# Kernel optimization log

Measured on AMD Instinct MI355X. Metric: run time of the kernel, lower is better.

Reference implementation:

```python
import jax, jax.numpy as jnp
import numpy as np

HID = 1024; INTER = 2048; NSTATE = 16; KCONV = 4; DTRANK = 64
NHEADS = 16; NKV = 4; HDIM = 64; VHDIM = 128; EPS = 1e-6
ATTN_H = HID; K_H = NKV * HDIM; V_H = NKV * VHDIM
LATENT = INTER + ATTN_H + K_H + V_H  # 3840


def rmsnorm(x, w, eps=EPS):
    return x * jax.lax.rsqrt(jnp.mean(x * x, axis=-1, keepdims=True) + eps) * w


def setup_inputs():
    key = jax.random.key(0)
    ks = jax.random.split(key, 8)
    B, S = 2, 2048
    s = 0.02
    x = jax.random.normal(ks[0], (B, S, HID), jnp.float32)
    W_in = jax.random.normal(ks[1], (LATENT + INTER, HID), jnp.float32) * s
    conv_w = jax.random.normal(ks[2], (INTER, KCONV), jnp.float32) * 0.2
    conv_b = jnp.zeros((INTER,), jnp.float32)
    W_x = jax.random.normal(ks[3], (DTRANK + 2 * NSTATE, INTER), jnp.float32) * s
    dt_ln_w = jnp.ones((DTRANK,), jnp.float32)
    B_ln_w = jnp.ones((NSTATE,), jnp.float32)
    C_ln_w = jnp.ones((NSTATE,), jnp.float32)
    W_dt = jax.random.normal(ks[4], (INTER, DTRANK), jnp.float32) * s
    b_dt = jnp.log(jnp.expm1(jnp.full((INTER,), 0.01, jnp.float32)))
    A_log = jnp.log(jnp.broadcast_to(jnp.arange(1, NSTATE + 1, dtype=jnp.float32)[None, :], (INTER, NSTATE)))
    D_param = jnp.ones((INTER,), jnp.float32)
    ln1_w = jnp.ones((INTER,), jnp.float32)
    ln2_w = jnp.ones((INTER,), jnp.float32)
    W_out = jax.random.normal(ks[5], (HID, INTER), jnp.float32) * s
    return {"x": x, "W_in": W_in, "conv_w": conv_w, "conv_b": conv_b, "W_x": W_x,
            "dt_ln_w": dt_ln_w, "B_ln_w": B_ln_w, "C_ln_w": C_ln_w, "W_dt": W_dt,
            "b_dt": b_dt, "A_log": A_log, "D_param": D_param, "ln1_w": ln1_w,
            "ln2_w": ln2_w, "W_out": W_out}


def reference(x, W_in, conv_w, conv_b, W_x, dt_ln_w, B_ln_w, C_ln_w, W_dt, b_dt,
              A_log, D_param, ln1_w, ln2_w, W_out):
    Bsz, S, _ = x.shape
    proj = x @ W_in.T  # [B,S,LATENT+INTER]
    q = proj[..., :ATTN_H]
    k = proj[..., ATTN_H:ATTN_H + K_H]
    v = proj[..., ATTN_H + K_H:ATTN_H + K_H + V_H]
    xs = proj[..., ATTN_H + K_H + V_H:LATENT]
    gate = proj[..., LATENT:]

    # depthwise causal conv1d + silu (causal_conv1d_fn)
    xt = xs.transpose(0, 2, 1)  # [B,D,S]
    xc = jax.lax.conv_general_dilated(xt, conv_w[:, None, :], (1,), [(KCONV - 1, 0)],
                                      feature_group_count=INTER,
                                      dimension_numbers=("NCH", "OIH", "NCH"))
    xc = jax.nn.silu(xc + conv_b[None, :, None]).transpose(0, 2, 1)  # [B,S,D]

    # input-dependent dt, B, C with inner RMSNorms
    ssm_p = xc @ W_x.T  # [B,S,DTRANK+2N]
    dt = rmsnorm(ssm_p[..., :DTRANK], dt_ln_w)
    Bm = rmsnorm(ssm_p[..., DTRANK:DTRANK + NSTATE], B_ln_w)
    Cm = rmsnorm(ssm_p[..., DTRANK + NSTATE:], C_ln_w)
    delta = jax.nn.softplus(dt @ W_dt.T + b_dt)  # [B,S,D] (delta_bias + softplus)
    A = -jnp.exp(A_log)  # [D,N]

    def step(h, inp):
        d_t, b_t, c_t, x_t = inp  # [B,D],[B,N],[B,N],[B,D]
        dA = jnp.exp(d_t[:, :, None] * A)  # [B,D,N]
        h = h * dA + (d_t * x_t)[:, :, None] * b_t[:, None, :]
        y = jnp.einsum("bdn,bn->bd", h, c_t)
        return h, y

    h0 = jnp.zeros((Bsz, INTER, NSTATE), x.dtype)
    _, ys = jax.lax.scan(step, h0, (delta.transpose(1, 0, 2), Bm.transpose(1, 0, 2),
                                    Cm.transpose(1, 0, 2), xc.transpose(1, 0, 2)))
    y = ys.transpose(1, 0, 2) + xc * D_param
    y = y * jax.nn.silu(gate)  # gated scan output [B,S,INTER]

    # causal GQA attention branch (no output proj; v_head_dim = INTER/NHEADS)
    qh = q.reshape(Bsz, S, NHEADS, HDIM).transpose(0, 2, 1, 3)
    kh = jnp.repeat(k.reshape(Bsz, S, NKV, HDIM), NHEADS // NKV, axis=2).transpose(0, 2, 1, 3)
    vh = jnp.repeat(v.reshape(Bsz, S, NKV, VHDIM), NHEADS // NKV, axis=2).transpose(0, 2, 1, 3)
    scores = jnp.einsum("bhqd,bhkd->bhqk", qh, kh) * (1.0 / float(np.sqrt(HDIM)))
    mask = jnp.tril(jnp.ones((S, S), bool))
    scores = jnp.where(mask, scores, jnp.finfo(scores.dtype).min)
    attn = jnp.einsum("bhqk,bhkd->bhqd", jax.nn.softmax(scores, axis=-1), vh)
    attn = attn.transpose(0, 2, 1, 3).reshape(Bsz, S, INTER)

    out = (rmsnorm(attn, ln1_w) + rmsnorm(y, ln2_w)) * 0.5
    return out @ W_out.T
```

## Files before the change

kernel.cpp:

```cpp
#include <hip/hip_runtime.h>
#include <stdint.h>

#define HID    1024
#define INTER  2048
#define NSTATE 16
#define DTRANK 64
#define NHEADS 16
#define NKV    4
#define HDIM   64
#define VHDIM  128
#define ATTN_H 1024
#define K_H    256
#define V_H    512
#define LATENT 3840
#define NCOLS  5888
#define BATCH  2
#define SEQ    2048
#define T_TOT  4096
#define NCHUNK 64
#define CHLEN  32

typedef __bf16 bf16x8 __attribute__((ext_vector_type(8)));
typedef float  f32x4  __attribute__((ext_vector_type(4)));
typedef float  f32x4v __attribute__((ext_vector_type(4)));
typedef unsigned short u16x8 __attribute__((ext_vector_type(8)));

__device__ __forceinline__ float bf2f(unsigned short u) {
    return __uint_as_float(((unsigned int)u) << 16);
}
__device__ __forceinline__ unsigned short f2bf(float f) {
    unsigned int u = __float_as_uint(f);
    u = (u + 0x7fffu + ((u >> 16) & 1u)) >> 16;
    return (unsigned short)u;
}
__device__ __forceinline__ bf16x8 ldb8(const unsigned short* p) {
    return __builtin_bit_cast(bf16x8, *(const u16x8*)p);
}

typedef const __attribute__((address_space(1))) unsigned int* gas_ptr;
typedef __attribute__((address_space(3))) unsigned int* las_ptr;
__device__ __forceinline__ void load_lds16(const void* g, void* l) {
    __builtin_amdgcn_global_load_lds((gas_ptr)g, (las_ptr)l, 16, 0, 0);
}

__global__ void k_cvt(const float* __restrict__ src, unsigned short* __restrict__ dst, int n8) {
    int i = blockIdx.x * blockDim.x + threadIdx.x;
    if (i >= n8) return;
    f32x4v a = ((const f32x4v*)src)[2 * i];
    f32x4v b = ((const f32x4v*)src)[2 * i + 1];
    u16x8 o;
#pragma unroll
    for (int k = 0; k < 4; k++) { o[k] = f2bf(a[k]); o[k + 4] = f2bf(b[k]); }
    *(u16x8*)(dst + (size_t)i * 8) = o;
}

__global__ void k_wxpad(const float* __restrict__ W_x, unsigned short* __restrict__ Wxpad) {
    int i = blockIdx.x * blockDim.x + threadIdx.x;
    int e = i * 8;
    int row = e >> 11;
    int col = e & 2047;
    u16x8 o;
    if (row < DTRANK + 2 * NSTATE) {
#pragma unroll
        for (int k = 0; k < 8; k++) o[k] = f2bf(W_x[(size_t)row * INTER + col + k]);
    } else {
#pragma unroll
        for (int k = 0; k < 8; k++) o[k] = 0;
    }
    *(u16x8*)(Wxpad + e) = o;
}

template <int OUT_MODE>
__launch_bounds__(256)
__global__ void k_gemm(const unsigned short* __restrict__ A, const unsigned short* __restrict__ B,
                       void* __restrict__ Cout, const float* __restrict__ bias,
                       int M, int N, int K, int lda, int ldb, int ldc) {
    __shared__ __align__(16) unsigned short As[128 * 64];
    __shared__ __align__(16) unsigned short Bs[128 * 64];
    const int tid = threadIdx.x;
    const int lane = tid & 63;
    const int w = tid >> 6;
    const int wm = w >> 1, wn = w & 1;
    const int bm = blockIdx.y * 128, bn = blockIdx.x * 128;

    f32x4 acc[4][4];
#pragma unroll
    for (int i = 0; i < 4; i++)
#pragma unroll
        for (int j = 0; j < 4; j++) acc[i][j] = (f32x4){0.f, 0.f, 0.f, 0.f};

    const int nk = K >> 6;
    for (int ks = 0; ks < nk; ++ks) {
        const int k0 = ks << 6;
#pragma unroll
        for (int i = 0; i < 4; ++i) {
            int qb = (w << 6) + (i << 8);
            int q = qb + lane;
            int row = q >> 3, c = q & 7;
            int csrc = c ^ (row & 7);
            load_lds16(A + (size_t)(bm + row) * lda + k0 + csrc * 8, As + qb * 8);
            load_lds16(B + (size_t)(bn + row) * ldb + k0 + csrc * 8, Bs + qb * 8);
        }
        __syncthreads();
#pragma unroll
        for (int kk = 0; kk < 2; ++kk) {
            bf16x8 af[4], bfr[4];
#pragma unroll
            for (int mi = 0; mi < 4; mi++) {
                int row = (wm << 6) + (mi << 4) + (lane & 15);
                int c = (kk << 2) + (lane >> 4);
                af[mi] = ldb8(As + row * 64 + (c ^ (row & 7)) * 8);
            }
#pragma unroll
            for (int ni = 0; ni < 4; ni++) {
                int row = (wn << 6) + (ni << 4) + (lane & 15);
                int c = (kk << 2) + (lane >> 4);
                bfr[ni] = ldb8(Bs + row * 64 + (c ^ (row & 7)) * 8);
            }
#pragma unroll
            for (int mi = 0; mi < 4; mi++)
#pragma unroll
                for (int ni = 0; ni < 4; ni++)
                    acc[mi][ni] = __builtin_amdgcn_mfma_f32_16x16x32_bf16(af[mi], bfr[ni], acc[mi][ni], 0, 0, 0);
        }
        __syncthreads();
    }
#pragma unroll
    for (int mi = 0; mi < 4; mi++)
#pragma unroll
        for (int ni = 0; ni < 4; ni++)
#pragma unroll
            for (int r = 0; r < 4; r++) {
                int grow = bm + (wm << 6) + (mi << 4) + ((lane >> 4) << 2) + r;
                int gcol = bn + (wn << 6) + (ni << 4) + (lane & 15);
                float v = acc[mi][ni][r];
                if (OUT_MODE == 0) {
                    ((unsigned short*)Cout)[(size_t)grow * ldc + gcol] = f2bf(v);
                } else if (OUT_MODE == 1) {
                    ((float*)Cout)[(size_t)grow * ldc + gcol] = v;
                } else {
                    v += bias[gcol];
                    v = (v > 20.f) ? v : log1pf(__expf(v));
                    ((unsigned short*)Cout)[(size_t)grow * ldc + gcol] = f2bf(v);
                }
            }
}

__global__ void k_conv(const unsigned short* __restrict__ proj, const float* __restrict__ conv_w,
                       const float* __restrict__ conv_b, unsigned short* __restrict__ xc) {
    int r = blockIdx.x;
    int d8 = threadIdx.x * 8;
    int t = r & (SEQ - 1);
    float accv[8];
#pragma unroll
    for (int i = 0; i < 8; i++) accv[i] = conv_b[d8 + i];
#pragma unroll
    for (int j = 0; j < 4; j++) {
        int tp = t - 3 + j;
        if (tp < 0) continue;
        u16x8 xv = *(const u16x8*)(proj + (size_t)(r - 3 + j) * NCOLS + (LATENT - INTER) + d8);
#pragma unroll
        for (int i = 0; i < 8; i++) accv[i] += conv_w[(d8 + i) * 4 + j] * bf2f(xv[i]);
    }
    u16x8 o;
#pragma unroll
    for (int i = 0; i < 8; i++) {
        float v = accv[i];
        v = v / (1.f + __expf(-v));
        o[i] = f2bf(v);
    }
    *(u16x8*)(xc + (size_t)r * INTER + d8) = o;
}

__global__ void k_rms3(const float* __restrict__ ssmp, const float* __restrict__ dt_w,
                       const float* __restrict__ B_w, const float* __restrict__ C_w,
                       unsigned short* __restrict__ dtbf, float* __restrict__ Bm, float* __restrict__ Cm) {
    int r = blockIdx.x;
    int tid = threadIdx.x;
    int lane = tid & 63, w = tid >> 6;
    int c = tid;
    float v = (c < 96) ? ssmp[(size_t)r * 128 + c] : 0.f;
    float s = v * v;
    if (w == 0) {
#pragma unroll
        for (int d = 1; d < 64; d <<= 1) s += __shfl_xor(s, d);
        float rms = rsqrtf(s * (1.f / 64.f) + 1e-6f);
        dtbf[(size_t)r * 64 + lane] = f2bf(v * rms * dt_w[lane]);
    } else {
#pragma unroll
        for (int d = 1; d < 16; d <<= 1) s += __shfl_xor(s, d);
        float rms = rsqrtf(s * (1.f / 16.f) + 1e-6f);
        if (lane < 16) Bm[(size_t)r * 16 + lane] = v * rms * B_w[lane];
        else if (lane < 32) Cm[(size_t)r * 16 + (lane - 16)] = v * rms * C_w[lane - 16];
    }
}

template <int PASS>
__launch_bounds__(256)
__global__ void k_scan_chunk(const unsigned short* __restrict__ deltabf, const unsigned short* __restrict__ xcbf,
                             const float* __restrict__ Bm, const float* __restrict__ Cm,
                             const float* __restrict__ A_log,
                             float* __restrict__ hend, float* __restrict__ sumd,
                             const float* __restrict__ hinit, unsigned short* __restrict__ ybf) {
    __shared__ __align__(16) unsigned short dltS[CHLEN * 256];
    __shared__ __align__(16) unsigned short xvS[CHLEN * 256];
    __shared__ __align__(16) float BsT[CHLEN * 16];
    __shared__ __align__(16) float CsT[CHLEN * 16];
    const int d0 = blockIdx.x * 256;
    const int c = blockIdx.y;
    const int b = blockIdx.z;
    const int tid = threadIdx.x, lane = tid & 63, w = tid >> 6;
    const int t0 = c * CHLEN;
    const size_t rowbase = (size_t)(b * SEQ + t0);

    float An[16];
    {
        const f32x4* ap = (const f32x4*)(A_log + (size_t)(d0 + tid) * 16);
#pragma unroll
        for (int n4 = 0; n4 < 4; n4++) {
            f32x4 av = ap[n4];
#pragma unroll
            for (int j = 0; j < 4; j++) An[n4 * 4 + j] = -__expf(av[j]);
        }
    }

#pragma unroll
    for (int i = 0; i < 4; ++i) {
        int qb = (w << 6) + (i << 8);
        int q = qb + lane;
        int t = q >> 5, coff = q & 31;
        load_lds16(deltabf + (rowbase + t) * INTER + d0 + coff * 8, dltS + qb * 8);
        load_lds16(xcbf + (rowbase + t) * INTER + d0 + coff * 8, xvS + qb * 8);
    }
    if (tid < 128) {
        ((f32x4*)BsT)[tid] = ((const f32x4*)(Bm + rowbase * 16))[tid];
        if (PASS == 2) ((f32x4*)CsT)[tid] = ((const f32x4*)(Cm + rowbase * 16))[tid];
    }
    __syncthreads();

    const size_t sidx = ((size_t)(c * BATCH + b) * INTER + d0 + tid) * 16;
    float h[16];
    if (PASS == 2) {
        const f32x4* hp = (const f32x4*)(hinit + sidx);
#pragma unroll
        for (int n4 = 0; n4 < 4; n4++) {
            f32x4 hv = hp[n4];
#pragma unroll
            for (int j = 0; j < 4; j++) h[n4 * 4 + j] = hv[j];
        }
    } else {
#pragma unroll
        for (int n = 0; n < 16; n++) h[n] = 0.f;
    }
    float sd = 0.f;
    for (int t = 0; t < CHLEN; ++t) {
        float dlt = bf2f(dltS[t * 256 + tid]);
        float xv = bf2f(xvS[t * 256 + tid]);
        float dx = dlt * xv;
        if (PASS == 0) sd += dlt;
        float y = 0.f;
#pragma unroll
        for (int n4 = 0; n4 < 4; ++n4) {
            f32x4 Bt = ((f32x4*)BsT)[t * 4 + n4];
            f32x4 Ct;
            if (PASS == 2) Ct = ((f32x4*)CsT)[t * 4 + n4];
#pragma unroll
            for (int j = 0; j < 4; ++j) {
                int n = n4 * 4 + j;
                float a = __expf(dlt * An[n]);
                h[n] = h[n] * a + dx * Bt[j];
                if (PASS == 2) y += h[n] * Ct[j];
            }
        }
        if (PASS == 2) ybf[(rowbase + t) * INTER + d0 + tid] = f2bf(y);
    }
    if (PASS == 0) {
        f32x4* hp = (f32x4*)(hend + sidx);
#pragma unroll
        for (int n4 = 0; n4 < 4; n4++) {
            f32x4 hv;
#pragma unroll
            for (int j = 0; j < 4; j++) hv[j] = h[n4 * 4 + j];
            hp[n4] = hv;
        }
        sumd[(size_t)(c * BATCH + b) * INTER + d0 + tid] = sd;
    }
}

__global__ void k_scan_prop(const float* __restrict__ A_log, const float* __restrict__ hend,
                            const float* __restrict__ sumd, float* __restrict__ hinit) {
    const int tid = blockIdx.x * 256 + threadIdx.x;
    const int n = tid & 15;
    const int d = (tid >> 4) & (INTER - 1);
    const float An = -__expf(A_log[(size_t)d * 16 + n]);
    const int bd = tid >> 4;
    float h = 0.f;
#pragma unroll 1
    for (int cb = 0; cb < NCHUNK / 4; ++cb) {
        float he[4], sdv[4];
#pragma unroll
        for (int j = 0; j < 4; j++) {
            int c = cb * 4 + j;
            he[j] = hend[(size_t)c * 65536 + tid];
            sdv[j] = sumd[(size_t)c * 4096 + bd];
        }
#pragma unroll
        for (int j = 0; j < 4; j++) {
            int c = cb * 4 + j;
            hinit[(size_t)c * 65536 + tid] = h;
            h = he[j] + __expf(An * sdv[j]) * h;
        }
    }
}

__launch_bounds__(256)
__global__ void k_attn(const unsigned short* __restrict__ proj, unsigned short* __restrict__ attn) {
    __shared__ __align__(16) unsigned short Ks[64 * 72];
    __shared__ __align__(16) unsigned short Vt[128 * 72];
    __shared__ __align__(16) unsigned short Ps[4 * 16 * 72];
    const int qt = (gridDim.x - 1) - blockIdx.x;
    const int h = blockIdx.y;
    const int b = blockIdx.z;
    const int g = h >> 2;
    const int tid = threadIdx.x, lane = tid & 63, w = tid >> 6;
    const int r0 = qt * 128;
    const int qw = r0 + w * 32;

    const int krow = tid >> 3, kc = tid & 7;
    const int kp2 = (tid & 31) * 2, vb = tid >> 5;

    const unsigned short* kbase = proj + (size_t)(b * SEQ) * NCOLS + ATTN_H + g * HDIM;
    const unsigned short* vbase = proj + (size_t)(b * SEQ) * NCOLS + (ATTN_H + K_H) + g * VHDIM;

    bf16x8 qf[2][2];
#pragma unroll
    for (int f = 0; f < 2; f++) {
        int qr = qw + f * 16 + (lane & 15);
        const unsigned short* qp = proj + (size_t)(b * SEQ + qr) * NCOLS + h * HDIM + ((lane >> 4) << 3);
        qf[f][0] = ldb8(qp);
        qf[f][1] = ldb8(qp + 32);
    }
    f32x4 O[2][8];
#pragma unroll
    for (int f = 0; f < 2; f++)
#pragma unroll
        for (int vf = 0; vf < 8; vf++) O[f][vf] = (f32x4){0.f, 0.f, 0.f, 0.f};
    float l_[2][4];
#pragma unroll
    for (int f = 0; f < 2; f++)
#pragma unroll
        for (int rg = 0; rg < 4; rg++) l_[f][rg] = 0.f;

    u16x8 krA[2], vrA[2][2], krB[2], vrB[2][2];

    auto LOAD = [&](u16x8* kr, u16x8 (*vr)[2], int kv) {
        const unsigned short* kp_ = kbase + (size_t)(kv + krow) * NCOLS + kc * 8;
        kr[0] = *(const u16x8*)kp_;
        kr[1] = *(const u16x8*)(kp_ + (size_t)32 * NCOLS);
        const unsigned short* vp_ = vbase + (size_t)(kv + kp2) * NCOLS + vb * 8;
        vr[0][0] = *(const u16x8*)vp_;
        vr[0][1] = *(const u16x8*)(vp_ + NCOLS);
        vr[1][0] = *(const u16x8*)(vp_ + 64);
        vr[1][1] = *(const u16x8*)(vp_ + NCOLS + 64);
    };
    auto WRITE = [&](u16x8* kr, u16x8 (*vr)[2]) {
        *(u16x8*)&Ks[krow * 72 + kc * 8] = kr[0];
        *(u16x8*)&Ks[(krow + 32) * 72 + kc * 8] = kr[1];
#pragma unroll
        for (int hf = 0; hf < 2; hf++) {
            u16x8 va = vr[hf][0], vb2 = vr[hf][1];
#pragma unroll
            for (int i = 0; i < 8; i++) {
                unsigned int pk = (unsigned int)va[i] | ((unsigned int)vb2[i] << 16);
                *(unsigned int*)&Vt[((vb + hf * 8) * 8 + i) * 72 + kp2] = pk;
            }
        }
    };
    auto COMPUTE = [&](int kv) {
        const int pbase = w * 16 * 72;
#pragma unroll
        for (int f = 0; f < 2; f++) {
            f32x4 sv[4];
#pragma unroll
            for (int cf = 0; cf < 4; ++cf) {
                f32x4 s = (f32x4){0.f, 0.f, 0.f, 0.f};
#pragma unroll
                for (int kk = 0; kk < 2; ++kk) {
                    bf16x8 kb = ldb8(&Ks[(cf * 16 + (lane & 15)) * 72 + kk * 32 + ((lane >> 4) << 3)]);
                    s = __builtin_amdgcn_mfma_f32_16x16x32_bf16(qf[f][kk], kb, s, 0, 0, 0);
                }
                sv[cf] = s;
            }
            const int qi0 = qw + f * 16 + ((lane >> 4) << 2);
#pragma unroll
            for (int cf = 0; cf < 4; ++cf) {
                int ki = kv + cf * 16 + (lane & 15);
#pragma unroll
                for (int rg = 0; rg < 4; ++rg) {
                    float v = (ki <= qi0 + rg) ? __expf(sv[cf][rg] * 0.125f) : 0.f;
                    l_[f][rg] += v;
                    Ps[pbase + (((lane >> 4) << 2) + rg) * 72 + cf * 16 + (lane & 15)] = f2bf(v);
                }
            }
            bf16x8 pa0 = ldb8(&Ps[pbase + (lane & 15) * 72 + ((lane >> 4) << 3)]);
            bf16x8 pa1 = ldb8(&Ps[pbase + (lane & 15) * 72 + 32 + ((lane >> 4) << 3)]);
#pragma unroll
            for (int vf = 0; vf < 8; ++vf) {
                bf16x8 v0 = ldb8(&Vt[(vf * 16 + (lane & 15)) * 72 + ((lane >> 4) << 3)]);
                bf16x8 v1 = ldb8(&Vt[(vf * 16 + (lane & 15)) * 72 + 32 + ((lane >> 4) << 3)]);
                O[f][vf] = __builtin_amdgcn_mfma_f32_16x16x32_bf16(pa0, v0, O[f][vf], 0, 0, 0);
                O[f][vf] = __builtin_amdgcn_mfma_f32_16x16x32_bf16(pa1, v1, O[f][vf], 0, 0, 0);
            }
        }
    };

    const int ntiles = 2 * (qt + 1);
    LOAD(krA, vrA, 0);
    for (int jj = 0; jj < ntiles; jj += 2) {
        WRITE(krA, vrA);
        LOAD(krB, vrB, (jj + 1) * 64);
        __syncthreads();
        COMPUTE(jj * 64);
        __syncthreads();
        WRITE(krB, vrB);
        if (jj + 2 < ntiles) LOAD(krA, vrA, (jj + 2) * 64);
        __syncthreads();
        COMPUTE((jj + 1) * 64);
        __syncthreads();
    }

#pragma unroll
    for (int f = 0; f < 2; f++) {
#pragma unroll
        for (int dd = 1; dd < 16; dd <<= 1)
#pragma unroll
            for (int rg = 0; rg < 4; ++rg) l_[f][rg] += __shfl_xor(l_[f][rg], dd);
#pragma unroll
        for (int rg = 0; rg < 4; ++rg) {
            float inv = 1.f / l_[f][rg];
            int grow = b * SEQ + qw + f * 16 + ((lane >> 4) << 2) + rg;
#pragma unroll
            for (int vf = 0; vf < 8; ++vf) {
                int gcol = h * VHDIM + vf * 16 + (lane & 15);
                attn[(size_t)grow * INTER + gcol] = f2bf(O[f][vf][rg] * inv);
            }
        }
    }
}

__launch_bounds__(256)
__global__ void k_fuse(const unsigned short* __restrict__ attn, const unsigned short* __restrict__ ybf,
                       const unsigned short* __restrict__ xc, const unsigned short* __restrict__ proj,
                       const float* __restrict__ Dp, const float* __restrict__ ln1,
                       const float* __restrict__ ln2, unsigned short* __restrict__ fused) {
    __shared__ float red[8];
    int r = blockIdx.x, tid = threadIdx.x;
    int c8 = tid * 8;
    u16x8 av = *(const u16x8*)(attn + (size_t)r * INTER + c8);
    u16x8 yv8 = *(const u16x8*)(ybf + (size_t)r * INTER + c8);
    u16x8 xv8 = *(const u16x8*)(xc + (size_t)r * INTER + c8);
    u16x8 gv8 = *(const u16x8*)(proj + (size_t)r * NCOLS + LATENT + c8);
    float a_[8], y_[8];
    float ssa = 0.f, ssy = 0.f;
#pragma unroll
    for (int i = 0; i < 8; i++) {
        float a = bf2f(av[i]);
        float yv = bf2f(yv8[i]) + bf2f(xv8[i]) * Dp[c8 + i];
        float gg = bf2f(gv8[i]);
        yv *= gg / (1.f + __expf(-gg));
        a_[i] = a; y_[i] = yv;
        ssa += a * a; ssy += yv * yv;
    }
#pragma unroll
    for (int d = 1; d < 64; d <<= 1) { ssa += __shfl_xor(ssa, d); ssy += __shfl_xor(ssy, d); }
    int w = tid >> 6, lane = tid & 63;
    if (lane == 0) { red[w * 2] = ssa; red[w * 2 + 1] = ssy; }
    __syncthreads();
    ssa = red[0] + red[2] + red[4] + red[6];
    ssy = red[1] + red[3] + red[5] + red[7];
    float ra = rsqrtf(ssa * (1.f / 2048.f) + 1e-6f);
    float ry = rsqrtf(ssy * (1.f / 2048.f) + 1e-6f);
    u16x8 o;
#pragma unroll
    for (int i = 0; i < 8; i++) {
        float v = (a_[i] * ra * ln1[c8 + i] + y_[i] * ry * ln2[c8 + i]) * 0.5f;
        o[i] = f2bf(v);
    }
    *(u16x8*)(fused + (size_t)r * INTER + c8) = o;
}

extern "C" void kernel_launch(void* const* d_in, const int* in_sizes, int n_in,
                              void* d_out, int out_size, void* d_ws, size_t ws_size,
                              hipStream_t stream) {
    const float* x      = (const float*)d_in[0];
    const float* W_in   = (const float*)d_in[1];
    const float* conv_w = (const float*)d_in[2];
    const float* conv_b = (const float*)d_in[3];
    const float* W_x    = (const float*)d_in[4];
    const float* dt_w   = (const float*)d_in[5];
    const float* B_w    = (const float*)d_in[6];
    const float* C_w    = (const float*)d_in[7];
    const float* W_dt   = (const float*)d_in[8];
    const float* b_dt   = (const float*)d_in[9];
    const float* A_log  = (const float*)d_in[10];
    const float* Dp     = (const float*)d_in[11];
    const float* ln1    = (const float*)d_in[12];
    const float* ln2    = (const float*)d_in[13];
    const float* W_out  = (const float*)d_in[14];
    float* out = (float*)d_out;

    char* p = (char*)d_ws;
    auto alloc = [&](size_t bytes) -> void* {
        void* r = (void*)p;
        p += (bytes + 255) & ~(size_t)255;
        return r;
    };
    unsigned short* xbf     = (unsigned short*)alloc((size_t)T_TOT * HID * 2);
    unsigned short* Winbf   = (unsigned short*)alloc((size_t)NCOLS * HID * 2);
    unsigned short* projbf  = (unsigned short*)alloc((size_t)T_TOT * NCOLS * 2);
    unsigned short* xcbf    = (unsigned short*)alloc((size_t)T_TOT * INTER * 2);
    unsigned short* Wxpad   = (unsigned short*)alloc((size_t)128 * INTER * 2);
    float*          ssmp    = (float*)alloc((size_t)T_TOT * 128 * 4);
    unsigned short* dtbf    = (unsigned short*)alloc((size_t)T_TOT * DTRANK * 2);
    float*          Bm      = (float*)alloc((size_t)T_TOT * 16 * 4);
    float*          Cm      = (float*)alloc((size_t)T_TOT * 16 * 4);
    unsigned short* Wdtbf   = (unsigned short*)alloc((size_t)INTER * DTRANK * 2);
    unsigned short* deltabf = (unsigned short*)alloc((size_t)T_TOT * INTER * 2);
    unsigned short* ybf     = (unsigned short*)alloc((size_t)T_TOT * INTER * 2);
    unsigned short* attnbf  = (unsigned short*)alloc((size_t)T_TOT * INTER * 2);
    unsigned short* fusedbf = (unsigned short*)alloc((size_t)T_TOT * INTER * 2);
    unsigned short* Woutbf  = (unsigned short*)alloc((size_t)HID * INTER * 2);
    float*          hendws  = (float*)alloc((size_t)NCHUNK * BATCH * INTER * 16 * 4);
    float*          hinitws = (float*)alloc((size_t)NCHUNK * BATCH * INTER * 16 * 4);
    float*          sumdws  = (float*)alloc((size_t)NCHUNK * BATCH * INTER * 4);

    k_cvt<<<(T_TOT * HID / 8 + 255) / 256, 256, 0, stream>>>(x, xbf, T_TOT * HID / 8);
    k_cvt<<<(NCOLS * HID / 8 + 255) / 256, 256, 0, stream>>>(W_in, Winbf, NCOLS * HID / 8);
    k_cvt<<<(INTER * DTRANK / 8 + 255) / 256, 256, 0, stream>>>(W_dt, Wdtbf, INTER * DTRANK / 8);
    k_cvt<<<(HID * INTER / 8 + 255) / 256, 256, 0, stream>>>(W_out, Woutbf, HID * INTER / 8);
    k_wxpad<<<(128 * INTER / 8) / 256, 256, 0, stream>>>(W_x, Wxpad);

    k_gemm<0><<<dim3(NCOLS / 128, T_TOT / 128), 256, 0, stream>>>(
        xbf, Winbf, projbf, nullptr, T_TOT, NCOLS, HID, HID, HID, NCOLS);
    k_conv<<<T_TOT, 256, 0, stream>>>(projbf, conv_w, conv_b, xcbf);
    k_gemm<1><<<dim3(1, T_TOT / 128), 256, 0, stream>>>(
        xcbf, Wxpad, ssmp, nullptr, T_TOT, 128, INTER, INTER, INTER, 128);
    k_rms3<<<T_TOT, 128, 0, stream>>>(ssmp, dt_w, B_w, C_w, dtbf, Bm, Cm);
    k_gemm<2><<<dim3(INTER / 128, T_TOT / 128), 256, 0, stream>>>(
        dtbf, Wdtbf, deltabf, b_dt, T_TOT, INTER, DTRANK, DTRANK, DTRANK, INTER);
    k_scan_chunk<0><<<dim3(INTER / 256, NCHUNK, BATCH), 256, 0, stream>>>(
        deltabf, xcbf, Bm, Cm, A_log, hendws, sumdws, nullptr, nullptr);
    k_scan_prop<<<256, 256, 0, stream>>>(A_log, hendws, sumdws, hinitws);
    k_scan_chunk<2><<<dim3(INTER / 256, NCHUNK, BATCH), 256, 0, stream>>>(
        deltabf, xcbf, Bm, Cm, A_log, nullptr, nullptr, hinitws, ybf);
    k_attn<<<dim3(SEQ / 128, NHEADS, BATCH), 256, 0, stream>>>(projbf, attnbf);
    k_fuse<<<T_TOT, 256, 0, stream>>>(attnbf, ybf, xcbf, projbf, Dp, ln1, ln2, fusedbf);
    k_gemm<1><<<dim3(HID / 128, T_TOT / 128), 256, 0, stream>>>(
        fusedbf, Woutbf, out, nullptr, T_TOT, HID, INTER, INTER, INTER, HID);
}
```

Baseline: 467.2 us.

## Split-K the x_proj GEMM and pair causal attention tiles per block

The thin x_proj GEMM (N=128, K=2048), which launched only 32 blocks, now runs as an 8-way split-K. Each split writes fp32 partials that the RMS-norm kernel sums. Attention now uses 64-row query tiles, and each block handles a complementary pair (31-p and p) so causal work is balanced across blocks. LDS K, V and P tiles switch from padded strides to XOR-swizzled layouts, and the softmax uses exp2 with a prescaled constant. The costs are extra partial-sum memory traffic and a smaller per-wave query tile.

```diff
diff --git a/kernel.cpp b/kernel.cpp
--- a/kernel.cpp
+++ b/kernel.cpp
@@ -82,6 +82,7 @@
     const int w = tid >> 6;
     const int wm = w >> 1, wn = w & 1;
     const int bm = blockIdx.y * 128, bn = blockIdx.x * 128;
+    const size_t koff = (OUT_MODE == 3) ? (size_t)blockIdx.z * K : 0;
 
     f32x4 acc[4][4];
 #pragma unroll
@@ -98,8 +99,8 @@
             int q = qb + lane;
             int row = q >> 3, c = q & 7;
             int csrc = c ^ (row & 7);
-            load_lds16(A + (size_t)(bm + row) * lda + k0 + csrc * 8, As + qb * 8);
-            load_lds16(B + (size_t)(bn + row) * ldb + k0 + csrc * 8, Bs + qb * 8);
+            load_lds16(A + (size_t)(bm + row) * lda + koff + k0 + csrc * 8, As + qb * 8);
+            load_lds16(B + (size_t)(bn + row) * ldb + koff + k0 + csrc * 8, Bs + qb * 8);
         }
         __syncthreads();
 #pragma unroll
@@ -138,6 +139,8 @@
                     ((unsigned short*)Cout)[(size_t)grow * ldc + gcol] = f2bf(v);
                 } else if (OUT_MODE == 1) {
                     ((float*)Cout)[(size_t)grow * ldc + gcol] = v;
+                } else if (OUT_MODE == 3) {
+                    ((float*)Cout)[(size_t)blockIdx.z * M * ldc + (size_t)grow * ldc + gcol] = v;
                 } else {
                     v += bias[gcol];
                     v = (v > 20.f) ? v : log1pf(__expf(v));
@@ -179,7 +182,11 @@
     int tid = threadIdx.x;
     int lane = tid & 63, w = tid >> 6;
     int c = tid;
-    float v = (c < 96) ? ssmp[(size_t)r * 128 + c] : 0.f;
+    float v = 0.f;
+    if (c < 96) {
+#pragma unroll
+        for (int s = 0; s < 8; s++) v += ssmp[(size_t)s * (T_TOT * 128) + (size_t)r * 128 + c];
+    }
     float s = v * v;
     if (w == 0) {
 #pragma unroll
@@ -315,41 +322,21 @@
 
 __launch_bounds__(256)
 __global__ void k_attn(const unsigned short* __restrict__ proj, unsigned short* __restrict__ attn) {
-    __shared__ __align__(16) unsigned short Ks[64 * 72];
-    __shared__ __align__(16) unsigned short Vt[128 * 72];
-    __shared__ __align__(16) unsigned short Ps[4 * 16 * 72];
-    const int qt = (gridDim.x - 1) - blockIdx.x;
+    __shared__ __align__(16) unsigned short Ks[64 * 64];
+    __shared__ __align__(16) unsigned short Vt[128 * 64];
+    __shared__ __align__(16) unsigned short Ps[4 * 16 * 64];
+    const int pair = blockIdx.x;
     const int h = blockIdx.y;
     const int b = blockIdx.z;
     const int g = h >> 2;
     const int tid = threadIdx.x, lane = tid & 63, w = tid >> 6;
-    const int r0 = qt * 128;
-    const int qw = r0 + w * 32;
+    const int l15 = lane & 15, hi = lane >> 4;
 
     const int krow = tid >> 3, kc = tid & 7;
     const int kp2 = (tid & 31) * 2, vb = tid >> 5;
 
     const unsigned short* kbase = proj + (size_t)(b * SEQ) * NCOLS + ATTN_H + g * HDIM;
     const unsigned short* vbase = proj + (size_t)(b * SEQ) * NCOLS + (ATTN_H + K_H) + g * VHDIM;
-
-    bf16x8 qf[2][2];
-#pragma unroll
-    for (int f = 0; f < 2; f++) {
-        int qr = qw + f * 16 + (lane & 15);
-        const unsigned short* qp = proj + (size_t)(b * SEQ + qr) * NCOLS + h * HDIM + ((lane >> 4) << 3);
-        qf[f][0] = ldb8(qp);
-        qf[f][1] = ldb8(qp + 32);
-    }
-    f32x4 O[2][8];
-#pragma unroll
-    for (int f = 0; f < 2; f++)
-#pragma unroll
-        for (int vf = 0; vf < 8; vf++) O[f][vf] = (f32x4){0.f, 0.f, 0.f, 0.f};
-    float l_[2][4];
-#pragma unroll
-    for (int f = 0; f < 2; f++)
-#pragma unroll
-        for (int rg = 0; rg < 4; rg++) l_[f][rg] = 0.f;
 
     u16x8 krA[2], vrA[2][2], krB[2], vrB[2][2];
 
@@ -364,85 +351,107 @@
         vr[1][1] = *(const u16x8*)(vp_ + NCOLS + 64);
     };
     auto WRITE = [&](u16x8* kr, u16x8 (*vr)[2]) {
-        *(u16x8*)&Ks[krow * 72 + kc * 8] = kr[0];
-        *(u16x8*)&Ks[(krow + 32) * 72 + kc * 8] = kr[1];
+        int ksw = (kc ^ (krow & 7)) << 3;
+        *(u16x8*)&Ks[krow * 64 + ksw] = kr[0];
+        *(u16x8*)&Ks[(krow + 32) * 64 + ksw] = kr[1];
 #pragma unroll
         for (int hf = 0; hf < 2; hf++) {
             u16x8 va = vr[hf][0], vb2 = vr[hf][1];
 #pragma unroll
             for (int i = 0; i < 8; i++) {
                 unsigned int pk = (unsigned int)va[i] | ((unsigned int)vb2[i] << 16);
-                *(unsigned int*)&Vt[((vb + hf * 8) * 8 + i) * 72 + kp2] = pk;
+                int r = (vb + hf * 8) * 8 + i;
+                *(unsigned int*)&Vt[r * 64 + (((kp2 >> 3) ^ (r & 7)) << 3) + (kp2 & 7)] = pk;
             }
         }
     };
-    auto COMPUTE = [&](int kv) {
-        const int pbase = w * 16 * 72;
-#pragma unroll
-        for (int f = 0; f < 2; f++) {
+
+    const float SC = 0.18033688f;
+
+    for (int phase = 0; phase < 2; ++phase) {
+        const int qt = (phase == 0) ? (31 - pair) : pair;
+        const int qw = qt * 64 + w * 16;
+        const int ntiles = qt + 1;
+
+        bf16x8 qf[2];
+        {
+            int qr = qw + l15;
+            const unsigned short* qp = proj + (size_t)(b * SEQ + qr) * NCOLS + h * HDIM + hi * 8;
+            qf[0] = ldb8(qp);
+            qf[1] = ldb8(qp + 32);
+        }
+        f32x4 O[8];
+#pragma unroll
+        for (int vf = 0; vf < 8; vf++) O[vf] = (f32x4){0.f, 0.f, 0.f, 0.f};
+        float l_[4] = {0.f, 0.f, 0.f, 0.f};
+
+        auto COMPUTE = [&](int kv) {
+            const int pbase = w * 1024;
             f32x4 sv[4];
 #pragma unroll
             for (int cf = 0; cf < 4; ++cf) {
                 f32x4 s = (f32x4){0.f, 0.f, 0.f, 0.f};
+                int row = cf * 16 + l15;
 #pragma unroll
                 for (int kk = 0; kk < 2; ++kk) {
-                    bf16x8 kb = ldb8(&Ks[(cf * 16 + (lane & 15)) * 72 + kk * 32 + ((lane >> 4) << 3)]);
-                    s = __builtin_amdgcn_mfma_f32_16x16x32_bf16(qf[f][kk], kb, s, 0, 0, 0);
+                    bf16x8 kb = ldb8(&Ks[row * 64 + ((((kk << 2) + hi) ^ (row & 7)) << 3)]);
+                    s = __builtin_amdgcn_mfma_f32_16x16x32_bf16(qf[kk], kb, s, 0, 0, 0);
                 }
                 sv[cf] = s;
             }
-            const int qi0 = qw + f * 16 + ((lane >> 4) << 2);
+            const int qi0 = qw + (hi << 2);
 #pragma unroll
             for (int cf = 0; cf < 4; ++cf) {
-                int ki = kv + cf * 16 + (lane & 15);
+                int ki = kv + cf * 16 + l15;
 #pragma unroll
                 for (int rg = 0; rg < 4; ++rg) {
-                    float v = (ki <= qi0 + rg) ? __expf(sv[cf][rg] * 0.125f) : 0.f;
-                    l_[f][rg] += v;
-                    Ps[pbase + (((lane >> 4) << 2) + rg) * 72 + cf * 16 + (lane & 15)] = f2bf(v);
+                    float v = (ki <= qi0 + rg) ? exp2f(sv[cf][rg] * SC) : 0.f;
+                    l_[rg] += v;
+                    int pr = (hi << 2) + rg;
+                    int pc = cf * 16 + l15;
+                    Ps[pbase + pr * 64 + (((pc >> 3) ^ (pr & 7)) << 3) + (pc & 7)] = f2bf(v);
                 }
             }
-            bf16x8 pa0 = ldb8(&Ps[pbase + (lane & 15) * 72 + ((lane >> 4) << 3)]);
-            bf16x8 pa1 = ldb8(&Ps[pbase + (lane & 15) * 72 + 32 + ((lane >> 4) << 3)]);
+            bf16x8 pa0 = ldb8(&Ps[pbase + l15 * 64 + ((hi ^ (l15 & 7)) << 3)]);
+            bf16x8 pa1 = ldb8(&Ps[pbase + l15 * 64 + (((4 + hi) ^ (l15 & 7)) << 3)]);
 #pragma unroll
             for (int vf = 0; vf < 8; ++vf) {
-                bf16x8 v0 = ldb8(&Vt[(vf * 16 + (lane & 15)) * 72 + ((lane >> 4) << 3)]);
-                bf16x8 v1 = ldb8(&Vt[(vf * 16 + (lane & 15)) * 72 + 32 + ((lane >> 4) << 3)]);
-                O[f][vf] = __builtin_amdgcn_mfma_f32_16x16x32_bf16(pa0, v0, O[f][vf], 0, 0, 0);
-                O[f][vf] = __builtin_amdgcn_mfma_f32_16x16x32_bf16(pa1, v1, O[f][vf], 0, 0, 0);
-            }
-        }
-    };
-
-    const int ntiles = 2 * (qt + 1);
-    LOAD(krA, vrA, 0);
-    for (int jj = 0; jj < ntiles; jj += 2) {
-        WRITE(krA, vrA);
-        LOAD(krB, vrB, (jj + 1) * 64);
-        __syncthreads();
-        COMPUTE(jj * 64);
-        __syncthreads();
-        WRITE(krB, vrB);
-        if (jj + 2 < ntiles) LOAD(krA, vrA, (jj + 2) * 64);
-        __syncthreads();
-        COMPUTE((jj + 1) * 64);
-        __syncthreads();
-    }
-
-#pragma unroll
-    for (int f = 0; f < 2; f++) {
+                int vr_ = vf * 16 + l15;
+                bf16x8 v0 = ldb8(&Vt[vr_ * 64 + ((hi ^ (vr_ & 7)) << 3)]);
+                bf16x8 v1 = ldb8(&Vt[vr_ * 64 + (((4 + hi) ^ (vr_ & 7)) << 3)]);
+                O[vf] = __builtin_amdgcn_mfma_f32_16x16x32_bf16(pa0, v0, O[vf], 0, 0, 0);
+                O[vf] = __builtin_amdgcn_mfma_f32_16x16x32_bf16(pa1, v1, O[vf], 0, 0, 0);
+            }
+        };
+
+        LOAD(krA, vrA, 0);
+        bool useA = true;
+        for (int j = 0; j < ntiles; ++j) {
+            if (useA) {
+                WRITE(krA, vrA);
+                if (j + 1 < ntiles) LOAD(krB, vrB, (j + 1) * 64);
+            } else {
+                WRITE(krB, vrB);
+                if (j + 1 < ntiles) LOAD(krA, vrA, (j + 1) * 64);
+            }
+            __syncthreads();
+            COMPUTE(j * 64);
+            __syncthreads();
+            useA = !useA;
+        }
+
 #pragma unroll
         for (int dd = 1; dd < 16; dd <<= 1)
 #pragma unroll
-            for (int rg = 0; rg < 4; ++rg) l_[f][rg] += __shfl_xor(l_[f][rg], dd);
+            for (int rg = 0; rg < 4; ++rg) l_[rg] += __shfl_xor(l_[rg], dd);
 #pragma unroll
         for (int rg = 0; rg < 4; ++rg) {
-            float inv = 1.f / l_[f][rg];
-            int grow = b * SEQ + qw + f * 16 + ((lane >> 4) << 2) + rg;
+            float inv = 1.f / l_[rg];
+            int grow = b * SEQ + qw + (hi << 2) + rg;
 #pragma unroll
             for (int vf = 0; vf < 8; ++vf) {
-                int gcol = h * VHDIM + vf * 16 + (lane & 15);
-                attn[(size_t)grow * INTER + gcol] = f2bf(O[f][vf][rg] * inv);
+                int gcol = h * VHDIM + vf * 16 + l15;
+                attn[(size_t)grow * INTER + gcol] = f2bf(O[vf][rg] * inv);
             }
         }
     }
@@ -520,7 +529,7 @@
     unsigned short* projbf  = (unsigned short*)alloc((size_t)T_TOT * NCOLS * 2);
     unsigned short* xcbf    = (unsigned short*)alloc((size_t)T_TOT * INTER * 2);
     unsigned short* Wxpad   = (unsigned short*)alloc((size_t)128 * INTER * 2);
-    float*          ssmp    = (float*)alloc((size_t)T_TOT * 128 * 4);
+    float*          ssmp    = (float*)alloc((size_t)8 * T_TOT * 128 * 4);
     unsigned short* dtbf    = (unsigned short*)alloc((size_t)T_TOT * DTRANK * 2);
     float*          Bm      = (float*)alloc((size_t)T_TOT * 16 * 4);
     float*          Cm      = (float*)alloc((size_t)T_TOT * 16 * 4);
@@ -543,8 +552,8 @@
     k_gemm<0><<<dim3(NCOLS / 128, T_TOT / 128), 256, 0, stream>>>(
         xbf, Winbf, projbf, nullptr, T_TOT, NCOLS, HID, HID, HID, NCOLS);
     k_conv<<<T_TOT, 256, 0, stream>>>(projbf, conv_w, conv_b, xcbf);
-    k_gemm<1><<<dim3(1, T_TOT / 128), 256, 0, stream>>>(
-        xcbf, Wxpad, ssmp, nullptr, T_TOT, 128, INTER, INTER, INTER, 128);
+    k_gemm<3><<<dim3(1, T_TOT / 128, 8), 256, 0, stream>>>(
+        xcbf, Wxpad, ssmp, nullptr, T_TOT, 128, 256, INTER, INTER, 128);
     k_rms3<<<T_TOT, 128, 0, stream>>>(ssmp, dt_w, B_w, C_w, dtbf, Bm, Cm);
     k_gemm<2><<<dim3(INTER / 128, T_TOT / 128), 256, 0, stream>>>(
         dtbf, Wdtbf, deltabf, b_dt, T_TOT, INTER, DTRANK, DTRANK, DTRANK, INTER);
@@ -553,7 +562,7 @@
     k_scan_prop<<<256, 256, 0, stream>>>(A_log, hendws, sumdws, hinitws);
     k_scan_chunk<2><<<dim3(INTER / 256, NCHUNK, BATCH), 256, 0, stream>>>(
         deltabf, xcbf, Bm, Cm, A_log, nullptr, nullptr, hinitws, ybf);
-    k_attn<<<dim3(SEQ / 128, NHEADS, BATCH), 256, 0, stream>>>(projbf, attnbf);
+    k_attn<<<dim3(16, NHEADS, BATCH), 256, 0, stream>>>(projbf, attnbf);
     k_fuse<<<T_TOT, 256, 0, stream>>>(attnbf, ybf, xcbf, projbf, Dp, ln1, ln2, fusedbf);
     k_gemm<1><<<dim3(HID / 128, T_TOT / 128), 256, 0, stream>>>(
         fusedbf, Woutbf, out, nullptr, T_TOT, HID, INTER, INTER, INTER, HID);
```

Result: faster. 406.7 us (-13.0%).
